# Optimization experiments

Hardware: AMD Instinct MI355X
Metric: run time of the kernel (lower is better)

The kernel has to match this reference:

```python
import jax, jax.numpy as jnp
import numpy as np

FTS, IN_DIM = 256, 255
U0, U1, DIM, EMB = 512, 256, 64, 512
BATCH = 256


def _fat_dense(x, w, b, act):
    # x: [fts, batch, in], w: [fts, in, out], b: [fts, out]
    y = jnp.einsum('fbi,fio->fbo', x, w) + b[:, None, :]
    return act(y)


def setup_inputs() -> dict:
    key = jax.random.key(0)
    ks = jax.random.split(key, 14)
    def w(k, shape, fan_in):
        return jax.random.normal(k, shape, dtype=jnp.float32) * (1.0 / np.sqrt(fan_in))
    inp = {
        'x': jax.random.uniform(ks[0], (BATCH, FTS, IN_DIM), dtype=jnp.float32),
        'w1': w(ks[1], (FTS, IN_DIM, U0), IN_DIM), 'b1': jnp.zeros((FTS, U0), jnp.float32),
        'w2': w(ks[2], (FTS, U0, U1), U0),        'b2': jnp.zeros((FTS, U1), jnp.float32),
        'w3': w(ks[3], (FTS, U1, DIM), U1),       'b3': jnp.zeros((FTS, DIM), jnp.float32),
        'codebook': jax.random.normal(ks[4], (EMB, DIM), dtype=jnp.float32),
        'w4': w(ks[5], (FTS, DIM, U1), DIM),      'b4': jnp.zeros((FTS, U1), jnp.float32),
        'w5': w(ks[6], (FTS, U1, U0), U1),        'b5': jnp.zeros((FTS, U0), jnp.float32),
        'w6': w(ks[7], (FTS, U0, FTS), U0),       'b6': jnp.zeros((FTS, FTS), jnp.float32),
    }
    return inp


def reference(x, w1, b1, w2, b2, w3, b3, codebook, w4, b4, w5, b5, w6, b6):
    relu, sig = jax.nn.relu, jax.nn.sigmoid
    h = jnp.transpose(x, (1, 0, 2))                      # [fts, batch, in]
    h = _fat_dense(h, w1, b1, relu)                      # [fts, batch, U0]
    h = _fat_dense(h, w2, b2, relu)                      # [fts, batch, U1]
    h = _fat_dense(h, w3, b3, relu)                      # [fts, batch, dim]
    # --- Vector quantization (EMA codebook, straight-through estimator) ---
    flat = h.reshape(-1, h.shape[-1])                    # [fts*batch, dim]
    d = (jnp.sum(flat * flat, axis=1, keepdims=True)
         - 2.0 * flat @ codebook.T
         + jnp.sum(codebook * codebook, axis=1))         # [fts*batch, emb]
    idx = jnp.argmin(d, axis=1)                          # [fts*batch]
    q = codebook[idx].reshape(h.shape)                   # [fts, batch, dim]
    q = h + jax.lax.stop_gradient(q - h)                 # straight-through
    # --- Decoder ---
    y = _fat_dense(q, w4, b4, relu)                      # [fts, batch, U1]
    y = _fat_dense(y, w5, b5, relu)                      # [fts, batch, U0]
    y = _fat_dense(y, w6, b6, sig)                       # [fts, batch, fts]
    return jnp.transpose(y, (1, 0, 2))                   # [batch, fts, fts]
```

## Files before the change

kernel.cpp:

```cpp
#include <hip/hip_runtime.h>
#include <hip/hip_bf16.h>
#include <math.h>

#define FTS 256
#define IN_DIM 255
#define U0 512
#define U1 256
#define DIM 64
#define EMB 512
#define BATCH 256

typedef __attribute__((ext_vector_type(4))) float f32x4;
typedef _Float16 half8 __attribute__((ext_vector_type(8)));

__device__ __forceinline__ int swz8(int x) { return (x ^ (x >> 3)) & 7; }

__device__ __forceinline__ int pswz(int k, int r) {
    return (k & ~63) | ((((k >> 3) & 7) ^ swz8(r)) << 3) | (k & 7);
}

__device__ __forceinline__ void gload16(void* lds, const void* g) {
    __builtin_amdgcn_global_load_lds(
        (const __attribute__((address_space(1))) unsigned int*)g,
        (__attribute__((address_space(3))) unsigned int*)lds, 16, 0, 0);
}

__global__ __launch_bounds__(256)
void split_x(const float* __restrict__ x, _Float16* __restrict__ Xh,
             _Float16* __restrict__ Xl) {
    const int R = blockIdx.x * 4 + (threadIdx.x >> 6);
    const int f = R >> 8, b = R & 255;
    const int kq = (threadIdx.x & 63) * 4;
    const float* src = x + ((size_t)b * FTS + f) * IN_DIM;
    _Float16 hb[4], lb[4];
#pragma unroll
    for (int i = 0; i < 4; i++) {
        int k = kq + i;
        float v = (k < IN_DIM) ? src[k] : 0.f;
        _Float16 h = (_Float16)v;
        hb[i] = h;
        lb[i] = (_Float16)((v - (float)h) * 4096.f);
    }
    size_t o = ((size_t)f * BATCH + b) * 256 + pswz(kq, b);
    *(uint2*)(Xh + o) = *(uint2*)hb;
    *(uint2*)(Xl + o) = *(uint2*)lb;
}

__global__ __launch_bounds__(256)
void cbk_prep(const float* __restrict__ cbk, _Float16* __restrict__ Ckh,
              _Float16* __restrict__ Ckl, float* __restrict__ cbn) {
    const int c = blockIdx.x * 256 + threadIdx.x;
    if (c >= EMB) return;
    const float* src = cbk + (size_t)c * 64;
    double s = 0.0;
#pragma unroll
    for (int i = 0; i < 8; i++) {
        float4 v0 = *(const float4*)(src + i * 8);
        float4 v1 = *(const float4*)(src + i * 8 + 4);
        float fv[8] = {v0.x, v0.y, v0.z, v0.w, v1.x, v1.y, v1.z, v1.w};
        _Float16 hv[8], lv[8];
#pragma unroll
        for (int e = 0; e < 8; e++) {
            float xx = fv[e];
            _Float16 hb = (_Float16)xx;
            hv[e] = hb;
            lv[e] = (_Float16)((xx - (float)hb) * 4096.f);
            s = fma((double)xx, (double)xx, s);
        }
        *(uint4*)(Ckh + (size_t)c * 64 + i * 8) = *(uint4*)hv;
        *(uint4*)(Ckl + (size_t)c * 64 + i * 8) = *(uint4*)lv;
    }
    cbn[c] = (float)s;
}

template<int ACT, int BN, int NBX_LOG2, bool OUT_TRANS, bool SPLIT_OUT, bool LO>
__global__ __launch_bounds__(256)
void sgemm(const _Float16* __restrict__ Ah, const _Float16* __restrict__ Al,
           const float* __restrict__ W, const float* __restrict__ bias,
           float* __restrict__ Cf, _Float16* __restrict__ Ch, _Float16* __restrict__ Cl,
           int M, int K, int KW, int N) {
    constexpr int NB = BN / 32;
    constexpr int WR = (BN == 128) ? 8 : 4;
    constexpr int BPF_LOG2 = NBX_LOG2 + 1;

    const int nwg = gridDim.x;
    const int bid = blockIdx.x;
    const int w   = (bid & 7) * (nwg >> 3) + (bid >> 3);
    const int f   = w >> BPF_LOG2;
    const int rem = w & ((1 << BPF_LOG2) - 1);
    const int bm  = (rem >> NBX_LOG2) * 128;
    const int bn  = (rem & ((1 << NBX_LOG2) - 1)) * BN;

    const int tid  = threadIdx.x;
    const int lane = tid & 63;
    const int wv   = tid >> 6;
    const int wr   = (wv >> 1) * 64;
    const int wc   = (wv & 1) * (BN / 2);
    const int kr   = lane & 15;
    const int kg   = lane >> 4;

    __shared__ _Float16 sAh[128 * 64];
    __shared__ _Float16 sAl[LO ? 128 * 64 : 8];
    __shared__ _Float16 sBh[BN * 64];
    __shared__ _Float16 sBl[LO ? BN * 64 : 8];

    f32x4 acc[4][NB] = {};
    f32x4 acx[4][NB] = {};

    const float* Wf = W + (size_t)f * KW * N;
    const _Float16* pAh = Ah + (size_t)f * M * K;
    const _Float16* pAl = LO ? Al + (size_t)f * M * K : nullptr;

    const int n0 = (BN == 128) ? (tid & 31) * 4 : (tid & 15) * 4;
    const int kb = (BN == 128) ? (tid >> 5) * 8 : (tid >> 4) * 4;
    float4 wreg[WR];

    auto stageA = [&](int k0) {
        if (LO) {
#pragma unroll
            for (int i = 0; i < 8; i++) {
                int gi = wv * 8 + i;
                const _Float16* base = (gi < 16) ? pAh : pAl;
                _Float16* dstb       = (gi < 16) ? sAh : sAl;
                int rowb = (gi & 15) * 8;
                const _Float16* src = base + (size_t)(bm + rowb + (lane >> 3)) * K
                                           + k0 + (lane & 7) * 8;
                gload16(dstb + rowb * 64, src);
            }
        } else {
#pragma unroll
            for (int i = 0; i < 4; i++) {
                int gi = wv * 4 + i;
                int rowb = gi * 8;
                const _Float16* src = pAh + (size_t)(bm + rowb + (lane >> 3)) * K
                                          + k0 + (lane & 7) * 8;
                gload16(sAh + rowb * 64, src);
            }
        }
    };
    auto loadW = [&](int k0) {
#pragma unroll
        for (int i = 0; i < WR; i++) {
            int k = k0 + kb + i;
            wreg[i] = (k < KW) ? *(const float4*)(Wf + (size_t)k * N + bn + n0)
                               : float4{0.f, 0.f, 0.f, 0.f};
        }
    };
    auto writeB = [&]() {
#pragma unroll
        for (int j = 0; j < 4; j++) {
            int n = n0 + j;
            _Float16 hv[WR], lv[WR];
#pragma unroll
            for (int i = 0; i < WR; i++) {
                float xx = ((const float*)&wreg[i])[j];
                _Float16 hb = (_Float16)xx;
                hv[i] = hb;
                if (LO) lv[i] = (_Float16)((xx - (float)hb) * 4096.f);
            }
            if (BN == 128) {
                int off = n * 64 + (((kb >> 3) ^ swz8(n)) << 3);
                *(uint4*)&sBh[off] = *(uint4*)hv;
                if (LO) *(uint4*)&sBl[off] = *(uint4*)lv;
            } else {
                int off = n * 64 + ((((kb >> 3) & 7) ^ swz8(n)) << 3) + (kb & 7);
                *(uint2*)&sBh[off] = *(uint2*)hv;
                if (LO) *(uint2*)&sBl[off] = *(uint2*)lv;
            }
        }
    };

    const int T = K / 64;

    stageA(0);
    loadW(0);
    __syncthreads();
    writeB();
    __syncthreads();

    for (int t = 0; t < T; t++) {
        const bool more = (t + 1 < T);
        if (more) loadW((t + 1) * 64);

#pragma unroll
        for (int kh = 0; kh < 2; kh++) {
            const int cb = kh * 4 + kg;
            half8 bh[NB], bl[NB];
#pragma unroll
            for (int nb = 0; nb < NB; nb++) {
                int n = wc + nb * 16 + kr;
                int off = n * 64 + ((cb ^ swz8(n)) << 3);
                bh[nb] = *(const half8*)&sBh[off];
                if (LO) bl[nb] = *(const half8*)&sBl[off];
            }
            __builtin_amdgcn_s_setprio(1);
#pragma unroll
            for (int rb = 0; rb < 4; rb++) {
                int m = wr + rb * 16 + kr;
                int off = m * 64 + ((cb ^ swz8(m)) << 3);
                half8 ah = *(const half8*)&sAh[off];
                half8 al;
                if (LO) al = *(const half8*)&sAl[off];
#pragma unroll
                for (int nb = 0; nb < NB; nb++) {
                    acc[rb][nb] = __builtin_amdgcn_mfma_f32_16x16x32_f16(ah, bh[nb], acc[rb][nb], 0, 0, 0);
                    if (LO) {
                        acx[rb][nb] = __builtin_amdgcn_mfma_f32_16x16x32_f16(ah, bl[nb], acx[rb][nb], 0, 0, 0);
                        acx[rb][nb] = __builtin_amdgcn_mfma_f32_16x16x32_f16(al, bh[nb], acx[rb][nb], 0, 0, 0);
                    }
                }
            }
            __builtin_amdgcn_s_setprio(0);
        }
        __syncthreads();
        if (more) {
            stageA((t + 1) * 64);
            writeB();
            __syncthreads();
        }
    }

#pragma unroll
    for (int nb = 0; nb < NB; nb++) {
        int col = bn + wc + nb * 16 + kr;
        float bval = bias[(size_t)f * N + col];
#pragma unroll
        for (int rb = 0; rb < 4; rb++) {
#pragma unroll
            for (int j = 0; j < 4; j++) {
                int row = bm + wr + rb * 16 + kg * 4 + j;
                float v = acc[rb][nb][j];
                if (LO) v += acx[rb][nb][j] * (1.0f / 4096.0f);
                v += bval;
                if (ACT == 0) v = v > 0.f ? v : 0.f;
                else          v = 1.f / (1.f + expf(-v));
                if (SPLIT_OUT) {
                    size_t o = ((size_t)f * M + row) * N + pswz(col, row);
                    _Float16 h = (_Float16)v;
                    Ch[o] = h;
                    if (LO) Cl[o] = (_Float16)((v - (float)h) * 4096.f);
                } else if (OUT_TRANS) {
                    Cf[(size_t)row * (FTS * FTS) + (size_t)f * N + col] = v;
                } else {
                    Cf[((size_t)f * M + row) * N + col] = v;
                }
            }
        }
    }
}

__global__ __launch_bounds__(256)
void l3_vq(const _Float16* __restrict__ Ah, const _Float16* __restrict__ Al,
           const float* __restrict__ W, const float* __restrict__ bias,
           const _Float16* __restrict__ Ckh, const _Float16* __restrict__ Ckl,
           const float* __restrict__ cbn, _Float16* __restrict__ Qh) {
    const int nwg = gridDim.x;
    const int bid = blockIdx.x;
    const int w   = (bid & 7) * (nwg >> 3) + (bid >> 3);
    const int f   = w >> 1;
    const int bm  = (w & 1) * 128;

    const int tid  = threadIdx.x;
    const int lane = tid & 63;
    const int wv   = tid >> 6;
    const int wr   = (wv >> 1) * 64;
    const int wch  = wv & 1;
    const int wc   = wch * 32;
    const int kr   = lane & 15;
    const int kg   = lane >> 4;

    __shared__ _Float16 sAh[128 * 64], sAl[128 * 64];
    __shared__ _Float16 sBh[64 * 64],  sBl[64 * 64];
    __shared__ float bd_s[2][128];
    __shared__ int   bi_s[2][128];

    f32x4 acc[4][2] = {};
    f32x4 acx[4][2] = {};

    const float* Wf = W + (size_t)f * U1 * DIM;
    const _Float16* pAh = Ah + (size_t)f * BATCH * U1;
    const _Float16* pAl = Al + (size_t)f * BATCH * U1;

    const int n0 = (tid & 15) * 4;
    const int kb = (tid >> 4) * 4;
    float4 wreg[4];

    auto stageA = [&](int k0) {
#pragma unroll
        for (int i = 0; i < 8; i++) {
            int gi = wv * 8 + i;
            const _Float16* base = (gi < 16) ? pAh : pAl;
            _Float16* dstb       = (gi < 16) ? sAh : sAl;
            int rowb = (gi & 15) * 8;
            const _Float16* src = base + (size_t)(bm + rowb + (lane >> 3)) * U1
                                       + k0 + (lane & 7) * 8;
            gload16(dstb + rowb * 64, src);
        }
    };
    auto loadW = [&](int k0) {
#pragma unroll
        for (int i = 0; i < 4; i++)
            wreg[i] = *(const float4*)(Wf + (size_t)(k0 + kb + i) * DIM + n0);
    };
    auto writeB = [&]() {
#pragma unroll
        for (int j = 0; j < 4; j++) {
            int n = n0 + j;
            _Float16 hv[4], lv[4];
#pragma unroll
            for (int i = 0; i < 4; i++) {
                float xx = ((const float*)&wreg[i])[j];
                _Float16 hb = (_Float16)xx;
                hv[i] = hb;
                lv[i] = (_Float16)((xx - (float)hb) * 4096.f);
            }
            int off = n * 64 + ((((kb >> 3) & 7) ^ swz8(n)) << 3) + (kb & 7);
            *(uint2*)&sBh[off] = *(uint2*)hv;
            *(uint2*)&sBl[off] = *(uint2*)lv;
        }
    };

    stageA(0);
    loadW(0);
    __syncthreads();
    writeB();
    __syncthreads();

    for (int t = 0; t < 4; t++) {
        const bool more = (t + 1 < 4);
        if (more) loadW((t + 1) * 64);
#pragma unroll
        for (int kh = 0; kh < 2; kh++) {
            const int cb = kh * 4 + kg;
            half8 bh[2], bl[2];
#pragma unroll
            for (int nb = 0; nb < 2; nb++) {
                int n = wc + nb * 16 + kr;
                int off = n * 64 + ((cb ^ swz8(n)) << 3);
                bh[nb] = *(const half8*)&sBh[off];
                bl[nb] = *(const half8*)&sBl[off];
            }
            __builtin_amdgcn_s_setprio(1);
#pragma unroll
            for (int rb = 0; rb < 4; rb++) {
                int m = wr + rb * 16 + kr;
                int off = m * 64 + ((cb ^ swz8(m)) << 3);
                half8 ah = *(const half8*)&sAh[off];
                half8 al = *(const half8*)&sAl[off];
#pragma unroll
                for (int nb = 0; nb < 2; nb++) {
                    acc[rb][nb] = __builtin_amdgcn_mfma_f32_16x16x32_f16(ah, bh[nb], acc[rb][nb], 0, 0, 0);
                    acx[rb][nb] = __builtin_amdgcn_mfma_f32_16x16x32_f16(ah, bl[nb], acx[rb][nb], 0, 0, 0);
                    acx[rb][nb] = __builtin_amdgcn_mfma_f32_16x16x32_f16(al, bh[nb], acx[rb][nb], 0, 0, 0);
                }
            }
            __builtin_amdgcn_s_setprio(0);
        }
        __syncthreads();
        if (more) {
            stageA((t + 1) * 64);
            writeB();
            __syncthreads();
        }
    }

#pragma unroll
    for (int nb = 0; nb < 2; nb++) {
        int col = wc + nb * 16 + kr;
        float bval = bias[(size_t)f * DIM + col];
#pragma unroll
        for (int rb = 0; rb < 4; rb++) {
#pragma unroll
            for (int j = 0; j < 4; j++) {
                int row = wr + rb * 16 + kg * 4 + j;
                float v = acc[rb][nb][j] + acx[rb][nb][j] * (1.0f / 4096.0f) + bval;
                v = v > 0.f ? v : 0.f;
                _Float16 h = (_Float16)v;
                int off = row * 64 + ((((col >> 3) & 7) ^ swz8(row)) << 3) + (col & 7);
                sAh[off] = h;
                sAl[off] = (_Float16)((v - (float)h) * 4096.f);
            }
        }
    }

    float bestv[4][4];
    int   bestid[4][4];
#pragma unroll
    for (int rb = 0; rb < 4; rb++)
#pragma unroll
        for (int j = 0; j < 4; j++) { bestv[rb][j] = 3.4e38f; bestid[rb][j] = 0; }

    for (int ct = 0; ct < 8; ct++) {
        __syncthreads();
        {
            const int c  = tid >> 2;
            const int kq = (tid & 3) * 16;
            const _Float16* s1 = Ckh + (size_t)(ct * 64 + c) * 64 + kq;
            const _Float16* s2 = Ckl + (size_t)(ct * 64 + c) * 64 + kq;
#pragma unroll
            for (int i = 0; i < 2; i++) {
                int dst = c * 64 + (((kq >> 3) + i) ^ swz8(c)) * 8;
                *(uint4*)&sBh[dst] = *(const uint4*)(s1 + i * 8);
                *(uint4*)&sBl[dst] = *(const uint4*)(s2 + i * 8);
            }
        }
        __syncthreads();

        f32x4 vacc[4][2] = {};
        f32x4 vacx[4][2] = {};
#pragma unroll
        for (int kh = 0; kh < 2; kh++) {
            const int cb = kh * 4 + kg;
            half8 ah[4], al[4], bh[2], bl[2];
#pragma unroll
            for (int rb = 0; rb < 4; rb++) {
                int m = wr + rb * 16 + kr;
                int off = m * 64 + (cb ^ swz8(m)) * 8;
                ah[rb] = *(const half8*)&sAh[off];
                al[rb] = *(const half8*)&sAl[off];
            }
#pragma unroll
            for (int nb = 0; nb < 2; nb++) {
                int n = wc + nb * 16 + kr;
                int off = n * 64 + (cb ^ swz8(n)) * 8;
                bh[nb] = *(const half8*)&sBh[off];
                bl[nb] = *(const half8*)&sBl[off];
            }
#pragma unroll
            for (int rb = 0; rb < 4; rb++)
#pragma unroll
                for (int nb = 0; nb < 2; nb++) {
                    vacc[rb][nb] = __builtin_amdgcn_mfma_f32_16x16x32_f16(ah[rb], bh[nb], vacc[rb][nb], 0, 0, 0);
                    vacx[rb][nb] = __builtin_amdgcn_mfma_f32_16x16x32_f16(ah[rb], bl[nb], vacx[rb][nb], 0, 0, 0);
                    vacx[rb][nb] = __builtin_amdgcn_mfma_f32_16x16x32_f16(al[rb], bh[nb], vacx[rb][nb], 0, 0, 0);
                }
        }
#pragma unroll
        for (int nb = 0; nb < 2; nb++) {
            int code = ct * 64 + wc + nb * 16 + kr;
            float cn = cbn[code];
#pragma unroll
            for (int rb = 0; rb < 4; rb++)
#pragma unroll
                for (int j = 0; j < 4; j++) {
                    float dot = vacc[rb][nb][j] + vacx[rb][nb][j] * (1.0f / 4096.0f);
                    float dist = fmaf(-2.f, dot, cn);
                    if (dist < bestv[rb][j]) { bestv[rb][j] = dist; bestid[rb][j] = code; }
                }
        }
    }

#pragma unroll
    for (int rb = 0; rb < 4; rb++)
#pragma unroll
        for (int j = 0; j < 4; j++) {
#pragma unroll
            for (int mask = 1; mask < 16; mask <<= 1) {
                float od = __shfl_xor(bestv[rb][j], mask, 64);
                int   oi = __shfl_xor(bestid[rb][j], mask, 64);
                if (od < bestv[rb][j] || (od == bestv[rb][j] && oi < bestid[rb][j])) {
                    bestv[rb][j] = od; bestid[rb][j] = oi;
                }
            }
            if (kr == 0) {
                int row = wr + rb * 16 + kg * 4 + j;
                bd_s[wch][row] = bestv[rb][j];
                bi_s[wch][row] = bestid[rb][j];
            }
        }
    __syncthreads();

    if (tid < 128) {
        float d0 = bd_s[0][tid], d1 = bd_s[1][tid];
        int   i0 = bi_s[0][tid], i1 = bi_s[1][tid];
        bi_s[0][tid] = (d1 < d0 || (d1 == d0 && i1 < i0)) ? i1 : i0;
    }
    __syncthreads();

    {
        const int r  = tid >> 1, hf = tid & 1;
        const int b  = bm + r;
        const int idx = bi_s[0][r];
#pragma unroll
        for (int ci = 0; ci < 4; ci++) {
            int g  = hf * 4 + ci;
            int ph = (g ^ swz8(b)) << 3;
            *(uint4*)&Qh[((size_t)f * BATCH + b) * 64 + ph] =
                *(const uint4*)&Ckh[(size_t)idx * 64 + g * 8];
        }
    }
}

extern "C" void kernel_launch(void* const* d_in, const int* in_sizes, int n_in,
                              void* d_out, int out_size, void* d_ws, size_t ws_size,
                              hipStream_t stream) {
    const float* x   = (const float*)d_in[0];
    const float* w1  = (const float*)d_in[1];
    const float* b1  = (const float*)d_in[2];
    const float* w2  = (const float*)d_in[3];
    const float* b2  = (const float*)d_in[4];
    const float* w3  = (const float*)d_in[5];
    const float* b3  = (const float*)d_in[6];
    const float* cbk = (const float*)d_in[7];
    const float* w4  = (const float*)d_in[8];
    const float* b4  = (const float*)d_in[9];
    const float* w5  = (const float*)d_in[10];
    const float* b5  = (const float*)d_in[11];
    const float* w6  = (const float*)d_in[12];
    const float* b6  = (const float*)d_in[13];
    float* out = (float*)d_out;

    char* P = (char*)d_ws;
    _Float16* Xh  = (_Float16*)(P);
    _Float16* Xl  = (_Float16*)(P + 33554432ull);
    _Float16* H1h = (_Float16*)(P + 67108864ull);
    _Float16* H1l = (_Float16*)(P + 134217728ull);
    _Float16* H2h = (_Float16*)(P + 201326592ull);
    _Float16* H2l = (_Float16*)(P + 234881024ull);
    _Float16* Qh  = (_Float16*)(P + 285212672ull);
    _Float16* Ckh = (_Float16*)(P + 301989888ull);
    _Float16* Ckl = (_Float16*)(P + 302055424ull);
    float*    cbn = (float*)   (P + 302120960ull);
    _Float16* Y1h = Xh;
    _Float16* Y2h = H1h;

    dim3 blk(256);

    split_x<<<dim3(16384), blk, 0, stream>>>(x, Xh, Xl);
    cbk_prep<<<dim3(2), blk, 0, stream>>>(cbk, Ckh, Ckl, cbn);

    sgemm<0, 128, 2, false, true,  true ><<<dim3(2048), blk, 0, stream>>>(Xh,  Xl,  w1, b1, nullptr, H1h, H1l, BATCH, 256, IN_DIM, U0);
    sgemm<0, 128, 1, false, true,  true ><<<dim3(1024), blk, 0, stream>>>(H1h, H1l, w2, b2, nullptr, H2h, H2l, BATCH, U0,  U0,     U1);
    l3_vq<<<dim3(512), blk, 0, stream>>>(H2h, H2l, w3, b3, Ckh, Ckl, cbn, Qh);
    sgemm<0, 128, 1, false, true,  false><<<dim3(1024), blk, 0, stream>>>(Qh,  nullptr, w4, b4, nullptr, Y1h, nullptr, BATCH, DIM, DIM, U1);
    sgemm<0, 128, 2, false, true,  false><<<dim3(2048), blk, 0, stream>>>(Y1h, nullptr, w5, b5, nullptr, Y2h, nullptr, BATCH, U1,  U1,  U0);
    sgemm<1, 128, 1, true,  false, false><<<dim3(1024), blk, 0, stream>>>(Y2h, nullptr, w6, b6, out,     nullptr, nullptr, BATCH, U0, U0, FTS);
}
```

Before: 446.4 us.

## Fuse decoder layer 4 GEMM into the layer-3 VQ kernel

The VQ kernel now writes the selected codebook rows into shared memory instead of global Qh. It then loads and converts the layer-4 weights to fp16 in LDS and runs the 64x256 GEMM with MFMA, applying bias and ReLU before writing the swizzled Y1h directly. This removes one kernel launch and the Qh global round trip. In exchange it adds LDS pressure (a larger sBh), more registers from the 4x8 accumulator tile, and scalar 2-byte stores in the epilogue.

```diff
diff --git a/kernel.cpp b/kernel.cpp
--- a/kernel.cpp
+++ b/kernel.cpp
@@ -250,10 +250,12 @@
 }
 
 __global__ __launch_bounds__(256)
-void l3_vq(const _Float16* __restrict__ Ah, const _Float16* __restrict__ Al,
-           const float* __restrict__ W, const float* __restrict__ bias,
-           const _Float16* __restrict__ Ckh, const _Float16* __restrict__ Ckl,
-           const float* __restrict__ cbn, _Float16* __restrict__ Qh) {
+void l3_vq4(const _Float16* __restrict__ Ah, const _Float16* __restrict__ Al,
+            const float* __restrict__ W, const float* __restrict__ bias,
+            const _Float16* __restrict__ Ckh, const _Float16* __restrict__ Ckl,
+            const float* __restrict__ cbn,
+            const float* __restrict__ W4, const float* __restrict__ b4,
+            _Float16* __restrict__ Y1h) {
     const int nwg = gridDim.x;
     const int bid = blockIdx.x;
     const int w   = (bid & 7) * (nwg >> 3) + (bid >> 3);
@@ -270,7 +272,8 @@
     const int kg   = lane >> 4;
 
     __shared__ _Float16 sAh[128 * 64], sAl[128 * 64];
-    __shared__ _Float16 sBh[64 * 64],  sBl[64 * 64];
+    __shared__ _Float16 sBh[256 * 64];
+    __shared__ _Float16 sBl[64 * 64];
     __shared__ float bd_s[2][128];
     __shared__ int   bi_s[2][128];
 
@@ -479,14 +482,78 @@
 
     {
         const int r  = tid >> 1, hf = tid & 1;
-        const int b  = bm + r;
         const int idx = bi_s[0][r];
 #pragma unroll
         for (int ci = 0; ci < 4; ci++) {
-            int g  = hf * 4 + ci;
-            int ph = (g ^ swz8(b)) << 3;
-            *(uint4*)&Qh[((size_t)f * BATCH + b) * 64 + ph] =
-                *(const uint4*)&Ckh[(size_t)idx * 64 + g * 8];
+            int g   = hf * 4 + ci;
+            int dst = r * 64 + ((g ^ swz8(r)) << 3);
+            *(uint4*)&sAh[dst] = *(const uint4*)&Ckh[(size_t)idx * 64 + g * 8];
+        }
+    }
+    {
+        const int nq = (tid & 63) * 4;
+        const int kq = (tid >> 6) * 16;
+        const float* W4f = W4 + (size_t)f * DIM * U1;
+        float4 rows[16];
+#pragma unroll
+        for (int i = 0; i < 16; i++)
+            rows[i] = *(const float4*)(W4f + (size_t)(kq + i) * U1 + nq);
+#pragma unroll
+        for (int j = 0; j < 4; j++) {
+            int n = nq + j;
+            _Float16 hv[16];
+#pragma unroll
+            for (int i = 0; i < 16; i++)
+                hv[i] = (_Float16)(((const float*)&rows[i])[j]);
+#pragma unroll
+            for (int i = 0; i < 2; i++) {
+                int dst = n * 64 + ((((kq >> 3) + i) ^ swz8(n)) << 3);
+                *(uint4*)&sBh[dst] = *(uint4*)&hv[i * 8];
+            }
+        }
+    }
+    __syncthreads();
+
+    {
+        const int wc4 = (wv & 1) * 128;
+        f32x4 dacc[4][8] = {};
+#pragma unroll
+        for (int kh = 0; kh < 2; kh++) {
+            const int cb = kh * 4 + kg;
+            half8 bh[8];
+#pragma unroll
+            for (int nb = 0; nb < 8; nb++) {
+                int n = wc4 + nb * 16 + kr;
+                int off = n * 64 + ((cb ^ swz8(n)) << 3);
+                bh[nb] = *(const half8*)&sBh[off];
+            }
+            __builtin_amdgcn_s_setprio(1);
+#pragma unroll
+            for (int rb = 0; rb < 4; rb++) {
+                int m = wr + rb * 16 + kr;
+                int off = m * 64 + ((cb ^ swz8(m)) << 3);
+                half8 ah = *(const half8*)&sAh[off];
+#pragma unroll
+                for (int nb = 0; nb < 8; nb++)
+                    dacc[rb][nb] = __builtin_amdgcn_mfma_f32_16x16x32_f16(ah, bh[nb], dacc[rb][nb], 0, 0, 0);
+            }
+            __builtin_amdgcn_s_setprio(0);
+        }
+#pragma unroll
+        for (int nb = 0; nb < 8; nb++) {
+            int col = wc4 + nb * 16 + kr;
+            float bval = b4[(size_t)f * U1 + col];
+#pragma unroll
+            for (int rb = 0; rb < 4; rb++) {
+#pragma unroll
+                for (int j = 0; j < 4; j++) {
+                    int brow = bm + wr + rb * 16 + kg * 4 + j;
+                    float v = dacc[rb][nb][j] + bval;
+                    v = v > 0.f ? v : 0.f;
+                    size_t o = ((size_t)f * BATCH + brow) * U1 + pswz(col, brow);
+                    Y1h[o] = (_Float16)v;
+                }
+            }
         }
     }
 }
@@ -517,11 +584,10 @@
     _Float16* H1l = (_Float16*)(P + 134217728ull);
     _Float16* H2h = (_Float16*)(P + 201326592ull);
     _Float16* H2l = (_Float16*)(P + 234881024ull);
-    _Float16* Qh  = (_Float16*)(P + 285212672ull);
+    _Float16* Y1h = (_Float16*)(P + 268435456ull);
     _Float16* Ckh = (_Float16*)(P + 301989888ull);
     _Float16* Ckl = (_Float16*)(P + 302055424ull);
     float*    cbn = (float*)   (P + 302120960ull);
-    _Float16* Y1h = Xh;
     _Float16* Y2h = H1h;
 
     dim3 blk(256);
@@ -531,8 +597,7 @@
 
     sgemm<0, 128, 2, false, true,  true ><<<dim3(2048), blk, 0, stream>>>(Xh,  Xl,  w1, b1, nullptr, H1h, H1l, BATCH, 256, IN_DIM, U0);
     sgemm<0, 128, 1, false, true,  true ><<<dim3(1024), blk, 0, stream>>>(H1h, H1l, w2, b2, nullptr, H2h, H2l, BATCH, U0,  U0,     U1);
-    l3_vq<<<dim3(512), blk, 0, stream>>>(H2h, H2l, w3, b3, Ckh, Ckl, cbn, Qh);
-    sgemm<0, 128, 1, false, true,  false><<<dim3(1024), blk, 0, stream>>>(Qh,  nullptr, w4, b4, nullptr, Y1h, nullptr, BATCH, DIM, DIM, U1);
+    l3_vq4<<<dim3(512), blk, 0, stream>>>(H2h, H2l, w3, b3, Ckh, Ckl, cbn, w4, b4, Y1h);
     sgemm<0, 128, 2, false, true,  false><<<dim3(2048), blk, 0, stream>>>(Y1h, nullptr, w5, b5, nullptr, Y2h, nullptr, BATCH, U1,  U1,  U0);
     sgemm<1, 128, 1, true,  false, false><<<dim3(1024), blk, 0, stream>>>(Y2h, nullptr, w6, b6, out,     nullptr, nullptr, BATCH, U0, U0, FTS);
 }
```

Result: slower. 461.5 us (+3.4%).
